# Optimization experiments

Measured on AMD Instinct MI355X. Metric: run time of the kernel, lower is better.

## Reference

```python
import jax, jax.numpy as jnp
import numpy as np

HEADS = 8
DIM_HEAD = 64
NB_FEATURES = 256
CHUNK = 128          # chunk size used by performer's causal_linear_attention_noncuda
EPS_KERNEL = 1e-4    # eps in softmax_kernel feature map
EPS_DENOM = 1e-6     # eps added to k_cumsum in the denominator


def softmax_kernel(data, proj, is_query):
    # FAVOR+ positive softmax random features (performer_pytorch.softmax_kernel)
    # data: [B,H,N,D], proj: [M,D]
    d = data.shape[-1]
    normalizer = d ** -0.25
    ratio = proj.shape[0] ** -0.5
    data_dash = jnp.einsum('bhnd,md->bhnm', data * normalizer, proj)
    # ||x||^2 / (2*sqrt(d))
    diag = jnp.sum(data * data, axis=-1, keepdims=True) * 0.5 * (normalizer ** 2)
    if is_query:
        m = jax.lax.stop_gradient(jnp.max(data_dash, axis=-1, keepdims=True))
    else:
        m = jax.lax.stop_gradient(jnp.max(data_dash, axis=(-1, -2), keepdims=True))
    return ratio * (jnp.exp(data_dash - diag - m) + EPS_KERNEL)


def causal_linear_attention(qp, kp, v, chunk=CHUNK):
    # Chunked causal linear attention (O(N) in seq len):
    # out_i = q'_i . S_i / (q'_i . z_i), S_i = sum_{j<=i} k'_j v_j^T, z_i = cumsum k'_j
    B, H, N, M = qp.shape
    E = v.shape[-1]
    C = N // chunk

    def to_chunks(x):
        return x.reshape(B, H, C, chunk, x.shape[-1]).transpose(2, 0, 1, 3, 4)

    qc, kc, vc = to_chunks(qp), to_chunks(kp), to_chunks(v)
    k0 = jnp.zeros((B, H, M), qp.dtype)
    s0 = jnp.zeros((B, H, M, E), qp.dtype)

    def step(carry, inp):
        k_last, s_last = carry
        q, k, vv = inp  # [B,H,c,M], [B,H,c,M], [B,H,c,E]
        k_cum = k_last[:, :, None, :] + jnp.cumsum(k, axis=2)           # [B,H,c,M]
        d_inv = 1.0 / jnp.einsum('bhnm,bhnm->bhn', q, k_cum + EPS_DENOM)
        ctx = jnp.einsum('bhnm,bhne->bhnme', k, vv)                      # [B,H,c,M,E]
        s_cum = s_last[:, :, None] + jnp.cumsum(ctx, axis=2)             # [B,H,c,M,E]
        out = jnp.einsum('bhnme,bhnm,bhn->bhne', s_cum, q, d_inv)        # [B,H,c,E]
        return (k_cum[:, :, -1, :], s_cum[:, :, -1]), out

    _, outs = jax.lax.scan(step, (k0, s0), (qc, kc, vc))  # [C,B,H,c,E]
    return outs.transpose(1, 2, 0, 3, 4).reshape(B, H, N, E)


def setup_inputs() -> dict:
    key = jax.random.key(0)
    k1, k2, k3, k4 = jax.random.split(key, 4)
    B, N, D = 4, 2048, 512
    return {
        'query': jax.random.normal(k1, (B, N, D), jnp.float32),
        'key': jax.random.normal(k2, (B, N, D), jnp.float32),
        'value': jax.random.normal(k3, (B, N, D), jnp.float32),
        'projection': jax.random.normal(k4, (NB_FEATURES, DIM_HEAD), jnp.float32),
    }


def reference(query, key, value, projection):
    B, N, D = query.shape

    def split(x):  # [B,N,D] -> [B,H,N,Dh]
        return x.reshape(B, N, HEADS, DIM_HEAD).transpose(0, 2, 1, 3)

    q, k, v = split(query), split(key), split(value)
    qp = softmax_kernel(q, projection, is_query=True)
    kp = softmax_kernel(k, projection, is_query=False)
    out = causal_linear_attention(qp, kp, v)
    return out.transpose(0, 2, 1, 3).reshape(B, N, D)
```

## Files before the change

### kernel.cpp

```cpp
#include <hip/hip_runtime.h>
#include <math.h>

#define BB 4
#define NN 2048
#define DD 512
#define HH 8
#define DH 64
#define MM 256
#define BH 32
#define CHK 128
#define NCH 16
#define ROWS (BH*NN)

constexpr float NRM   = 0.35355339059327373f;
constexpr float RATIO = 0.0625f;
constexpr float EPSK  = 1e-4f;
constexpr float EPSD  = 1e-6f;
constexpr float REPS  = 0.0625f * 1e-4f;

#define OFFB_QP   ((size_t)0)
#define OFFB_SP   ((size_t)33554432)
#define OFFB_KP   (OFFB_SP + (size_t)16777216)
#define OFFB_VT   (OFFB_KP + (size_t)33554432)
#define OFFB_Z    (OFFB_VT + (size_t)8388608)
#define OFFB_KMP  (OFFB_Z  + (size_t)524288)
#define OFFB_G    (OFFB_KMP + (size_t)4096)

typedef __attribute__((ext_vector_type(8))) short short8;
typedef __attribute__((ext_vector_type(4))) float f32x4;

__device__ __forceinline__ float b2f(ushort u) {
  union { float f; unsigned int i; } x; x.i = ((unsigned int)u) << 16; return x.f;
}
__device__ __forceinline__ ushort f2b(float f) {
  unsigned int u = __float_as_uint(f);
  unsigned int r = (u + 0x7FFFu + ((u >> 16) & 1u)) >> 16;
  return (ushort)r;
}

#define MFMA(a,b,c) __builtin_amdgcn_mfma_f32_16x16x32_bf16(a, b, c, 0, 0, 0)

template<int MODE>
__device__ __forceinline__ void featm_body(const float* __restrict__ inp,
                                           const float* __restrict__ proj,
                                           char* __restrict__ ws,
                                           char* lds, int blk) {
  ushort* xh = (ushort*)lds;
  ushort* xl = xh + 64*72;
  ushort* qt = (ushort*)lds;
  float* diag_s = (float*)(lds + 33792);
  float (*wmax)[4] = (float(*)[4])(lds + 34048);
  float* kred = (float*)(lds + 35072);

  const int t  = threadIdx.x;
  const int w  = t >> 6;
  const int l  = t & 63;
  const int lq = l >> 4;
  const int ln = l & 15;

  const int rowbase = blk * 64;
  const int bh = rowbase >> 11;
  const int b  = bh >> 3, h = bh & 7;
  const int n0 = rowbase & (NN - 1);

  {
    const int r  = t >> 2;
    const int c0 = (t & 3) * 16;
    const float* src = inp + ((size_t)(b*NN + n0 + r))*DD + h*DH + c0;
    float vv[16];
    #pragma unroll
    for (int j = 0; j < 4; ++j) {
      float4 v = *(const float4*)(src + j*4);
      vv[4*j+0] = v.x*NRM; vv[4*j+1] = v.y*NRM;
      vv[4*j+2] = v.z*NRM; vv[4*j+3] = v.w*NRM;
    }
    float s = 0.f;
    ushort hi[16], lo[16];
    #pragma unroll
    for (int j = 0; j < 16; ++j) {
      s += vv[j]*vv[j];
      hi[j] = f2b(vv[j]);
      lo[j] = f2b(vv[j] - b2f(hi[j]));
    }
    *(short8*)(xh + r*72 + c0)     = *(short8*)&hi[0];
    *(short8*)(xh + r*72 + c0 + 8) = *(short8*)&hi[8];
    *(short8*)(xl + r*72 + c0)     = *(short8*)&lo[0];
    *(short8*)(xl + r*72 + c0 + 8) = *(short8*)&lo[8];
    s += __shfl_xor(s, 1); s += __shfl_xor(s, 2);
    if ((t & 3) == 0) diag_s[r] = 0.5f * s;
  }

  short8 bfr[2][2][2];
  #pragma unroll
  for (int p = 0; p < 2; ++p)
    #pragma unroll
    for (int ntl = 0; ntl < 2; ++ntl) {
      const float* pr = proj + (size_t)(p*128 + w*32 + ntl*16 + ln)*DH;
      #pragma unroll
      for (int kk = 0; kk < 2; ++kk) {
        float4 f0 = *(const float4*)(pr + kk*32 + lq*8);
        float4 f1 = *(const float4*)(pr + kk*32 + lq*8 + 4);
        ushort u[8] = {f2b(f0.x), f2b(f0.y), f2b(f0.z), f2b(f0.w),
                       f2b(f1.x), f2b(f1.y), f2b(f1.z), f2b(f1.w)};
        bfr[p][ntl][kk] = *(short8*)&u[0];
      }
    }

  f32x4 acc[4][4];
  #pragma unroll
  for (int mt = 0; mt < 4; ++mt)
    #pragma unroll
    for (int c = 0; c < 4; ++c) acc[mt][c] = (f32x4){0.f,0.f,0.f,0.f};

  __syncthreads();

  #pragma unroll
  for (int kk = 0; kk < 2; ++kk) {
    short8 ah[4], al[4];
    #pragma unroll
    for (int mt = 0; mt < 4; ++mt) {
      ah[mt] = *(const short8*)(xh + (mt*16 + ln)*72 + kk*32 + lq*8);
      al[mt] = *(const short8*)(xl + (mt*16 + ln)*72 + kk*32 + lq*8);
    }
    #pragma unroll
    for (int p = 0; p < 2; ++p)
      #pragma unroll
      for (int ntl = 0; ntl < 2; ++ntl) {
        short8 bf = bfr[p][ntl][kk];
        #pragma unroll
        for (int mt = 0; mt < 4; ++mt) {
          acc[mt][2*p+ntl] = MFMA(al[mt], bf, acc[mt][2*p+ntl]);
          acc[mt][2*p+ntl] = MFMA(ah[mt], bf, acc[mt][2*p+ntl]);
        }
      }
  }

  if (MODE == 0) {
    #pragma unroll
    for (int mt = 0; mt < 4; ++mt)
      #pragma unroll
      for (int reg = 0; reg < 4; ++reg) {
        float m = acc[mt][0][reg];
        #pragma unroll
        for (int c = 1; c < 4; ++c) m = fmaxf(m, acc[mt][c][reg]);
        m = fmaxf(m, __shfl_xor(m, 1));
        m = fmaxf(m, __shfl_xor(m, 2));
        m = fmaxf(m, __shfl_xor(m, 4));
        m = fmaxf(m, __shfl_xor(m, 8));
        if (ln == 0) wmax[mt*16 + lq*4 + reg][w] = m;
      }
  } else {
    float mx = -1e30f;
    #pragma unroll
    for (int mt = 0; mt < 4; ++mt)
      #pragma unroll
      for (int c = 0; c < 4; ++c)
        #pragma unroll
        for (int reg = 0; reg < 4; ++reg) mx = fmaxf(mx, acc[mt][c][reg]);
    #pragma unroll
    for (int m = 1; m < 64; m <<= 1) mx = fmaxf(mx, __shfl_xor(mx, m));
    if (l == 0) kred[w] = mx;
  }
  __syncthreads();

  float km = 0.f;
  if (MODE == 1) {
    km = fmaxf(fmaxf(kred[0], kred[1]), fmaxf(kred[2], kred[3]));
    if (t == 0) ((float*)(ws + OFFB_KMP))[blk] = km;
  }

  #pragma unroll
  for (int mt = 0; mt < 4; ++mt)
    #pragma unroll
    for (int reg = 0; reg < 4; ++reg) {
      const int row = mt*16 + lq*4 + reg;
      float rm;
      if (MODE == 0) {
        float4 wm4 = *(const float4*)&wmax[row][0];
        rm = fmaxf(fmaxf(wm4.x, wm4.y), fmaxf(wm4.z, wm4.w));
      } else {
        rm = km;
      }
      const float dg = diag_s[row];
      #pragma unroll
      for (int c = 0; c < 4; ++c) {
        const int f = (c >> 1)*128 + w*32 + (c & 1)*16 + ln;
        const float e = __expf(acc[mt][c][reg] - dg - rm);
        qt[row*264 + f] = f2b(MODE == 0 ? RATIO*(e + EPSK) : e);
      }
    }
  __syncthreads();

  ushort* dstbase = (ushort*)(ws + (MODE == 0 ? OFFB_QP : OFFB_KP)) + (size_t)rowbase*MM;
  #pragma unroll
  for (int ld = 0; ld < 8; ++ld) {
    int flat = t + 256*ld;
    int row = flat >> 5, g = flat & 31;
    *(short8*)(dstbase + (size_t)row*MM + g*8) = *(const short8*)(qt + row*264 + g*8);
  }
}

__device__ __forceinline__ void vt_body(const float* __restrict__ value,
                                        char* __restrict__ ws,
                                        char* lds, int blk) {
  float (*vsh)[68] = (float(*)[68])lds;
  const int t = threadIdx.x;
  const int bh = blk >> 4, nc = blk & 15;
  const int b = bh >> 3, h = bh & 7;
  const int n0 = nc * CHK;
  #pragma unroll
  for (int l = 0; l < 8; ++l) {
    int flat = t + 256*l;
    int r = flat >> 4, g = flat & 15;
    *(float4*)&vsh[r][g*4] = *(const float4*)(value + ((size_t)(b*NN + n0 + r))*DD + h*DH + g*4);
  }
  __syncthreads();
  const int e = t & 63, qd = t >> 6;
  ushort* vt = (ushort*)(ws + OFFB_VT) + ((size_t)bh*DH + e)*NN + n0 + qd*32;
  #pragma unroll
  for (int p = 0; p < 16; ++p) {
    unsigned int lo = f2b(vsh[qd*32 + 2*p][e]);
    unsigned int hi = f2b(vsh[qd*32 + 2*p + 1][e]);
    ((unsigned int*)vt)[p] = lo | (hi << 16);
  }
}

__global__ __launch_bounds__(256) void mega_kernel(const float* __restrict__ q,
                                                   const float* __restrict__ k,
                                                   const float* __restrict__ v,
                                                   const float* __restrict__ proj,
                                                   char* __restrict__ ws) {
  __shared__ __align__(16) char lds[35088];
  const int blk = blockIdx.x;
  if (blk < 1024)       featm_body<0>(q, proj, ws, lds, blk);
  else if (blk < 2048)  featm_body<1>(k, proj, ws, lds, blk - 1024);
  else                  vt_body(v, ws, lds, blk - 2048);
}

__global__ __launch_bounds__(256) void gchunk_kernel(char* __restrict__ ws) {
  __shared__ __align__(16) unsigned int kpTh[128*68];
  __shared__ __align__(16) ushort Vts[64*136];

  const int t  = threadIdx.x;
  const int w  = t >> 6;
  const int l  = t & 63;
  const int lq = l >> 4;
  const int ln = l & 15;

  const int blk = blockIdx.x;
  const int mh  = blk & 1;
  const int tc  = (blk >> 1) & 15;
  const int bh  = blk >> 5;

  const float* kmp = (const float*)(ws + OFFB_KMP) + bh*32;
  float km = kmp[0];
  #pragma unroll
  for (int i = 1; i < 32; ++i) km = fmaxf(km, kmp[i]);

  ushort* kpc = (ushort*)(ws + OFFB_KP) + ((size_t)bh*NN + (size_t)tc*CHK)*MM + mh*128;
  const ushort* vtb = (const ushort*)(ws + OFFB_VT) + (size_t)bh*DH*NN + tc*CHK;

  #pragma unroll
  for (int it = 0; it < 4; ++it) {
    int flat = t + 256*it;
    int jp = flat >> 4, mg = flat & 15;
    const float s0 = RATIO * __expf(kmp[tc*2 + (jp >> 5)] - km);
    short8 a = *(const short8*)(kpc + (size_t)(2*jp)*MM + mg*8);
    short8 c = *(const short8*)(kpc + (size_t)(2*jp+1)*MM + mg*8);
    ushort ua[8], uc[8];
    #pragma unroll
    for (int i = 0; i < 8; ++i) {
      ua[i] = f2b(fmaf(b2f((ushort)a[i]), s0, REPS));
      uc[i] = f2b(fmaf(b2f((ushort)c[i]), s0, REPS));
    }
    #pragma unroll
    for (int i = 0; i < 8; ++i)
      kpTh[(mg*8 + i)*68 + jp] = (unsigned int)ua[i] | ((unsigned int)uc[i] << 16);
    *(short8*)(kpc + (size_t)(2*jp)*MM + mg*8)   = *(short8*)&ua[0];
    *(short8*)(kpc + (size_t)(2*jp+1)*MM + mg*8) = *(short8*)&uc[0];
  }
  #pragma unroll
  for (int it = 0; it < 4; ++it) {
    int slot = t + 256*it;
    int e = slot >> 4, g = slot & 15;
    *(short8*)(Vts + e*136 + g*8) = *(const short8*)(vtb + (size_t)e*NN + g*8);
  }
  __syncthreads();

  {
    int m = t >> 1, half = t & 1;
    float s = 0.f;
    #pragma unroll
    for (int u = 0; u < 32; ++u) {
      unsigned int p = kpTh[m*68 + half*32 + u];
      s += b2f((ushort)(p & 0xFFFF)) + b2f((ushort)(p >> 16));
    }
    s += __shfl_xor(s, 1);
    if (half == 0)
      ((float*)(ws + OFFB_Z))[((size_t)bh*NCH + tc)*MM + mh*128 + m] = s;
  }

  f32x4 acc[8];
  #pragma unroll
  for (int nt = 0; nt < 8; ++nt) acc[nt] = (f32x4){0.f,0.f,0.f,0.f};
  short8 af[4];
  #pragma unroll
  for (int kk = 0; kk < 4; ++kk)
    af[kk] = *(const short8*)(Vts + (w*16 + ln)*136 + kk*32 + lq*8);
  #pragma unroll
  for (int nt = 0; nt < 8; ++nt)
    #pragma unroll
    for (int kk = 0; kk < 4; ++kk) {
      short8 bf = *(const short8*)((const ushort*)kpTh + (size_t)(nt*16 + ln)*136 + kk*32 + lq*8);
      acc[nt] = MFMA(af[kk], bf, acc[nt]);
    }

  float* gb = (float*)(ws + OFFB_G) + ((size_t)bh*NCH + tc)*DH*MM + mh*128;
  #pragma unroll
  for (int nt = 0; nt < 8; ++nt)
    #pragma unroll
    for (int reg = 0; reg < 4; ++reg)
      gb[(size_t)(w*16 + lq*4 + reg)*MM + nt*16 + ln] = acc[nt][reg];
}

__global__ __launch_bounds__(256) void scan_kernel(char* __restrict__ ws) {
  const int t  = threadIdx.x;
  const int bh = blockIdx.x / 17;
  const int sl = blockIdx.x % 17;
  if (sl < 16) {
    const int e  = sl*4 + (t >> 6);
    const int m4 = (t & 63) * 4;
    const float* gb = (const float*)(ws + OFFB_G) + ((size_t)bh*NCH*DH + e)*MM + m4;
    ushort*     spb = (ushort*)(ws + OFFB_SP)     + ((size_t)bh*NCH*DH + e)*MM + m4;
    float4 g[NCH];
    #pragma unroll
    for (int tc = 0; tc < NCH; ++tc)
      g[tc] = *(const float4*)(gb + (size_t)tc*DH*MM);
    float4 acc = {0.f, 0.f, 0.f, 0.f};
    #pragma unroll
    for (int tc = 0; tc < NCH; ++tc) {
      ushort4 o;
      o.x = f2b(acc.x); o.y = f2b(acc.y); o.z = f2b(acc.z); o.w = f2b(acc.w);
      *(ushort4*)(spb + (size_t)tc*DH*MM) = o;
      acc.x += g[tc].x; acc.y += g[tc].y; acc.z += g[tc].z; acc.w += g[tc].w;
    }
  } else {
    float* zf = (float*)(ws + OFFB_Z) + (size_t)bh*NCH*MM + t;
    float g[NCH];
    #pragma unroll
    for (int tc = 0; tc < NCH; ++tc) g[tc] = zf[(size_t)tc*MM];
    float acc = 0.f;
    #pragma unroll
    for (int tc = 0; tc < NCH; ++tc) { zf[(size_t)tc*MM] = acc; acc += g[tc]; }
  }
}

__global__ __launch_bounds__(256) void fused_kernel(float* __restrict__ out,
                                                    char* __restrict__ ws) {
  __shared__ __align__(16) char lds[52224];
  __shared__ float den_i[128];
  __shared__ float dinv_s[128];

  const int t  = threadIdx.x;
  const int w  = t >> 6;
  const int l  = t & 63;
  const int lq = l >> 4;
  const int ln = l & 15;
  const int rt0 = w;
  const int rt1 = 7 - w;
  const int blk = blockIdx.x;
  const int bh = blk >> 4, tc = blk & 15;
  const int b = bh >> 3, h = bh & 7;
  const size_t rowbase = (size_t)bh*NN + tc*CHK;

  const ushort* qpg = (const ushort*)(ws + OFFB_QP) + rowbase*MM;
  const ushort* kpg = (const ushort*)(ws + OFFB_KP) + rowbase*MM;
  const ushort* spg = (const ushort*)(ws + OFFB_SP) + (size_t)blk*DH*MM;

  ushort* qs = (ushort*)lds;
  ushort* ks = qs + 128*72;
  ushort* ss = ks + 128*72;

  f32x4 acc[2][8];
  #pragma unroll
  for (int mt = 0; mt < 2; ++mt)
    #pragma unroll
    for (int nt = 0; nt < 8; ++nt) acc[mt][nt] = (f32x4){0.f,0.f,0.f,0.f};
  f32x4 oacc[2][4];
  #pragma unroll
  for (int mt = 0; mt < 2; ++mt)
    #pragma unroll
    for (int nt = 0; nt < 4; ++nt) oacc[mt][nt] = (f32x4){0.f,0.f,0.f,0.f};

  for (int mc = 0; mc < 4; ++mc) {
    __syncthreads();
    #pragma unroll
    for (int ld2 = 0; ld2 < 4; ++ld2) {
      int flat = t + 256*ld2; int r = flat >> 3, g = flat & 7;
      *(short8*)(qs + r*72 + g*8) = *(const short8*)(qpg + (size_t)r*MM + mc*64 + g*8);
    }
    #pragma unroll
    for (int ld2 = 0; ld2 < 4; ++ld2) {
      int flat = t + 256*ld2; int r = flat >> 3, g = flat & 7;
      *(short8*)(ks + r*72 + g*8) = *(const short8*)(kpg + (size_t)r*MM + mc*64 + g*8);
    }
    #pragma unroll
    for (int ld2 = 0; ld2 < 2; ++ld2) {
      int flat = t + 256*ld2; int e = flat >> 3, g = flat & 7;
      *(short8*)(ss + e*72 + g*8) = *(const short8*)(spg + (size_t)e*MM + mc*64 + g*8);
    }
    __syncthreads();
    #pragma unroll
    for (int kk = 0; kk < 2; ++kk) {
      short8 af0 = *(const short8*)(qs + (rt0*16 + ln)*72 + kk*32 + lq*8);
      short8 af1 = *(const short8*)(qs + (rt1*16 + ln)*72 + kk*32 + lq*8);
      #pragma unroll
      for (int nt = 0; nt < 8; ++nt) {
        if (nt <= rt1) {
          short8 bf = *(const short8*)(ks + (nt*16 + ln)*72 + kk*32 + lq*8);
          if (nt <= rt0) acc[0][nt] = MFMA(af0, bf, acc[0][nt]);
          acc[1][nt] = MFMA(af1, bf, acc[1][nt]);
        }
      }
      #pragma unroll
      for (int nt = 0; nt < 4; ++nt) {
        short8 bf = *(const short8*)(ss + (nt*16 + ln)*72 + kk*32 + lq*8);
        oacc[0][nt] = MFMA(af0, bf, oacc[0][nt]);
        oacc[1][nt] = MFMA(af1, bf, oacc[1][nt]);
      }
    }
  }

  __syncthreads();

  ushort* P   = (ushort*)lds;
  ushort* Vts = (ushort*)(lds + 34816);

  float rs[2][4] = {{0,0,0,0},{0,0,0,0}};
  #pragma unroll
  for (int mt = 0; mt < 2; ++mt) {
    const int ibase = (mt ? rt1 : rt0) * 16;
    #pragma unroll
    for (int nt = 0; nt < 8; ++nt)
      #pragma unroll
      for (int reg = 0; reg < 4; ++reg) {
        int i = ibase + lq*4 + reg;
        int j = nt*16 + ln;
        float v = (j <= i) ? acc[mt][nt][reg] : 0.f;
        rs[mt][reg] += v;
        P[i*136 + j] = f2b(v);
      }
  }
  #pragma unroll
  for (int mt = 0; mt < 2; ++mt) {
    const int ibase = (mt ? rt1 : rt0) * 16;
    #pragma unroll
    for (int reg = 0; reg < 4; ++reg) {
      float s = rs[mt][reg];
      s += __shfl_xor(s, 1); s += __shfl_xor(s, 2);
      s += __shfl_xor(s, 4); s += __shfl_xor(s, 8);
      if (ln == 0) den_i[ibase + lq*4 + reg] = s;
    }
  }

  const ushort* vtg = (const ushort*)(ws + OFFB_VT) + (size_t)bh*DH*NN + tc*CHK;
  #pragma unroll
  for (int ld2 = 0; ld2 < 4; ++ld2) {
    int flat = t + 256*ld2; int e = flat >> 4, g = flat & 15;
    *(short8*)(Vts + e*136 + g*8) = *(const short8*)(vtg + (size_t)e*NN + g*8);
  }
  __syncthreads();

  {
    const float* zp = (const float*)(ws + OFFB_Z) + (size_t)blk*MM;
    const int r = t >> 1, hf = t & 1;
    const ushort* qrow = qpg + (size_t)r*MM + hf*128;
    float s = 0.f;
    #pragma unroll
    for (int g = 0; g < 16; ++g) {
      short8 qv = *(const short8*)(qrow + g*8);
      const float* zz = zp + hf*128 + g*8;
      #pragma unroll
      for (int x = 0; x < 8; ++x)
        s += b2f((ushort)qv[x]) * (zz[x] + EPSD);
    }
    s += __shfl_xor(s, 1);
    if (hf == 0) dinv_s[r] = 1.0f / (s + den_i[r]);
  }
  __syncthreads();

  #pragma unroll
  for (int kk = 0; kk < 4; ++kk) {
    short8 af0 = *(const short8*)(P + (rt0*16 + ln)*136 + kk*32 + lq*8);
    short8 af1 = *(const short8*)(P + (rt1*16 + ln)*136 + kk*32 + lq*8);
    #pragma unroll
    for (int nt = 0; nt < 4; ++nt) {
      short8 bf = *(const short8*)(Vts + (nt*16 + ln)*136 + kk*32 + lq*8);
      oacc[0][nt] = MFMA(af0, bf, oacc[0][nt]);
      oacc[1][nt] = MFMA(af1, bf, oacc[1][nt]);
    }
  }

  #pragma unroll
  for (int mt = 0; mt < 2; ++mt) {
    const int ibase = (mt ? rt1 : rt0) * 16;
    #pragma unroll
    for (int reg = 0; reg < 4; ++reg) {
      const int i = ibase + lq*4 + reg;
      const float di = dinv_s[i];
      float* dst = out + ((size_t)(b*NN) + tc*CHK + i)*DD + h*DH;
      #pragma unroll
      for (int nt = 0; nt < 4; ++nt)
        dst[nt*16 + ln] = oacc[mt][nt][reg] * di;
    }
  }
}

extern "C" void kernel_launch(void* const* d_in, const int* in_sizes, int n_in,
                              void* d_out, int out_size, void* d_ws, size_t ws_size,
                              hipStream_t stream) {
  (void)in_sizes; (void)n_in; (void)out_size; (void)ws_size;
  const float* q    = (const float*)d_in[0];
  const float* k    = (const float*)d_in[1];
  const float* v    = (const float*)d_in[2];
  const float* proj = (const float*)d_in[3];
  float* out = (float*)d_out;
  char*  ws  = (char*)d_ws;

  mega_kernel<<<2560, 256, 0, stream>>>(q, k, v, proj, ws);
  gchunk_kernel<<<1024, 256, 0, stream>>>(ws);
  scan_kernel<<<544, 256, 0, stream>>>(ws);
  fused_kernel<<<512, 256, 0, stream>>>(out, ws);
}
```

Measured before the change: 187.5 us.

## Drop scaled k' writeback, rescale in fused kernel, prefetch tiles into registers

The earlier kernel no longer writes the max-rescaled bf16 k' back to global memory. Instead, the fused kernel recomputes the per-chunk scale from the stored maxima and applies it while staging k' into LDS. The fused kernel also prefetches the next q/k/S column slice into registers during the MFMA loop, giving software pipelining of global loads. It computes the q·z denominator during staging, reusing loaded q values instead of re-reading q' from global memory. This removes global write and read traffic but adds register pressure, which may lower occupancy.

After: 168.3 us. 10.2% less time.

```diff
diff --git a/kernel.cpp b/kernel.cpp
--- a/kernel.cpp
+++ b/kernel.cpp
@@ -257,7 +257,7 @@
   #pragma unroll
   for (int i = 1; i < 32; ++i) km = fmaxf(km, kmp[i]);
 
-  ushort* kpc = (ushort*)(ws + OFFB_KP) + ((size_t)bh*NN + (size_t)tc*CHK)*MM + mh*128;
+  const ushort* kpc = (const ushort*)(ws + OFFB_KP) + ((size_t)bh*NN + (size_t)tc*CHK)*MM + mh*128;
   const ushort* vtb = (const ushort*)(ws + OFFB_VT) + (size_t)bh*DH*NN + tc*CHK;
 
   #pragma unroll
@@ -276,8 +276,6 @@
     #pragma unroll
     for (int i = 0; i < 8; ++i)
       kpTh[(mg*8 + i)*68 + jp] = (unsigned int)ua[i] | ((unsigned int)uc[i] << 16);
-    *(short8*)(kpc + (size_t)(2*jp)*MM + mg*8)   = *(short8*)&ua[0];
-    *(short8*)(kpc + (size_t)(2*jp+1)*MM + mg*8) = *(short8*)&uc[0];
   }
   #pragma unroll
   for (int it = 0; it < 4; ++it) {
@@ -359,6 +357,7 @@
                                                     char* __restrict__ ws) {
   __shared__ __align__(16) char lds[52224];
   __shared__ float den_i[128];
+  __shared__ float den_q[128];
   __shared__ float dinv_s[128];
 
   const int t  = threadIdx.x;
@@ -377,9 +376,38 @@
   const ushort* kpg = (const ushort*)(ws + OFFB_KP) + rowbase*MM;
   const ushort* spg = (const ushort*)(ws + OFFB_SP) + (size_t)blk*DH*MM;
 
+  const float* kmp = (const float*)(ws + OFFB_KMP) + bh*32;
+  float km = kmp[0];
+  #pragma unroll
+  for (int i = 1; i < 32; ++i) km = fmaxf(km, kmp[i]);
+  const float sc0 = RATIO * __expf(kmp[tc*2]     - km);
+  const float sc1 = RATIO * __expf(kmp[tc*2 + 1] - km);
+
   ushort* qs = (ushort*)lds;
   ushort* ks = qs + 128*72;
   ushort* ss = ks + 128*72;
+  float*  zl = (float*)(lds + 46080);
+
+  {
+    const float* zp = (const float*)(ws + OFFB_Z) + (size_t)blk*MM;
+    zl[t] = zp[t] + EPSD;
+  }
+
+  const int r4 = t >> 3;
+  const int g8 = t & 7;
+
+  short8 rq[4], rk[4], rs2[2];
+  #pragma unroll
+  for (int ld2 = 0; ld2 < 4; ++ld2)
+    rq[ld2] = *(const short8*)(qpg + (size_t)(r4 + 32*ld2)*MM + g8*8);
+  #pragma unroll
+  for (int ld2 = 0; ld2 < 4; ++ld2)
+    rk[ld2] = *(const short8*)(kpg + (size_t)(r4 + 32*ld2)*MM + g8*8);
+  #pragma unroll
+  for (int ld2 = 0; ld2 < 2; ++ld2)
+    rs2[ld2] = *(const short8*)(spg + (size_t)(r4 + 32*ld2)*MM + g8*8);
+
+  float dp[4] = {0.f, 0.f, 0.f, 0.f};
 
   f32x4 acc[2][8];
   #pragma unroll
@@ -396,20 +424,39 @@
     __syncthreads();
     #pragma unroll
     for (int ld2 = 0; ld2 < 4; ++ld2) {
-      int flat = t + 256*ld2; int r = flat >> 3, g = flat & 7;
-      *(short8*)(qs + r*72 + g*8) = *(const short8*)(qpg + (size_t)r*MM + mc*64 + g*8);
+      const int r = r4 + 32*ld2;
+      *(short8*)(qs + r*72 + g8*8) = rq[ld2];
+      #pragma unroll
+      for (int i = 0; i < 8; ++i)
+        dp[ld2] += b2f((ushort)rq[ld2][i]) * zl[mc*64 + g8*8 + i];
     }
     #pragma unroll
     for (int ld2 = 0; ld2 < 4; ++ld2) {
-      int flat = t + 256*ld2; int r = flat >> 3, g = flat & 7;
-      *(short8*)(ks + r*72 + g*8) = *(const short8*)(kpg + (size_t)r*MM + mc*64 + g*8);
-    }
-    #pragma unroll
-    for (int ld2 = 0; ld2 < 2; ++ld2) {
-      int flat = t + 256*ld2; int e = flat >> 3, g = flat & 7;
-      *(short8*)(ss + e*72 + g*8) = *(const short8*)(spg + (size_t)e*MM + mc*64 + g*8);
-    }
+      const int r = r4 + 32*ld2;
+      const float sc = (r & 64) ? sc1 : sc0;
+      ushort ov[8];
+      #pragma unroll
+      for (int i = 0; i < 8; ++i) ov[i] = f2b(fmaf(b2f((ushort)rk[ld2][i]), sc, REPS));
+      *(short8*)(ks + r*72 + g8*8) = *(short8*)&ov[0];
+    }
+    #pragma unroll
+    for (int ld2 = 0; ld2 < 2; ++ld2)
+      *(short8*)(ss + (r4 + 32*ld2)*72 + g8*8) = rs2[ld2];
     __syncthreads();
+
+    if (mc < 3) {
+      const int c0 = (mc + 1) * 64;
+      #pragma unroll
+      for (int ld2 = 0; ld2 < 4; ++ld2)
+        rq[ld2] = *(const short8*)(qpg + (size_t)(r4 + 32*ld2)*MM + c0 + g8*8);
+      #pragma unroll
+      for (int ld2 = 0; ld2 < 4; ++ld2)
+        rk[ld2] = *(const short8*)(kpg + (size_t)(r4 + 32*ld2)*MM + c0 + g8*8);
+      #pragma unroll
+      for (int ld2 = 0; ld2 < 2; ++ld2)
+        rs2[ld2] = *(const short8*)(spg + (size_t)(r4 + 32*ld2)*MM + c0 + g8*8);
+    }
+
     #pragma unroll
     for (int kk = 0; kk < 2; ++kk) {
       short8 af0 = *(const short8*)(qs + (rt0*16 + ln)*72 + kk*32 + lq*8);
@@ -431,6 +478,13 @@
     }
   }
 
+  #pragma unroll
+  for (int ld2 = 0; ld2 < 4; ++ld2) {
+    float s = dp[ld2];
+    s += __shfl_xor(s, 1); s += __shfl_xor(s, 2); s += __shfl_xor(s, 4);
+    if (g8 == 0) den_q[r4 + 32*ld2] = s;
+  }
+
   __syncthreads();
 
   ushort* P   = (ushort*)lds;
@@ -471,22 +525,7 @@
   }
   __syncthreads();
 
-  {
-    const float* zp = (const float*)(ws + OFFB_Z) + (size_t)blk*MM;
-    const int r = t >> 1, hf = t & 1;
-    const ushort* qrow = qpg + (size_t)r*MM + hf*128;
-    float s = 0.f;
-    #pragma unroll
-    for (int g = 0; g < 16; ++g) {
-      short8 qv = *(const short8*)(qrow + g*8);
-      const float* zz = zp + hf*128 + g*8;
-      #pragma unroll
-      for (int x = 0; x < 8; ++x)
-        s += b2f((ushort)qv[x]) * (zz[x] + EPSD);
-    }
-    s += __shfl_xor(s, 1);
-    if (hf == 0) dinv_s[r] = 1.0f / (s + den_i[r]);
-  }
+  if (t < 128) dinv_s[t] = 1.0f / (den_q[t] + den_i[t]);
   __syncthreads();
 
   #pragma unroll
```

## Fuse key rescaling into attention kernel, widen to 512 threads, prefetch tiles

Applied to the files above, without the earlier changes.

Stops gchunk_kernel from writing the rescaled bf16 key features back to global memory. fused_kernel now applies the per-chunk scale to keys while staging them into LDS. fused_kernel moves to 512 threads with one 16-row tile per wave, register-prefetches the next q/k/S slices during MFMA work, and folds the query·z denominator into the staging loop. mega_kernel gets an occupancy hint. This removes a global write pass and the separate denominator pass, at the cost of redundant scaling work and higher register pressure.

Result: faster. 174.5 us (-7.0%).

```diff
diff --git a/kernel.cpp b/kernel.cpp
--- a/kernel.cpp
+++ b/kernel.cpp
@@ -225,11 +225,11 @@
   }
 }
 
-__global__ __launch_bounds__(256) void mega_kernel(const float* __restrict__ q,
-                                                   const float* __restrict__ k,
-                                                   const float* __restrict__ v,
-                                                   const float* __restrict__ proj,
-                                                   char* __restrict__ ws) {
+__global__ __launch_bounds__(256, 3) void mega_kernel(const float* __restrict__ q,
+                                                      const float* __restrict__ k,
+                                                      const float* __restrict__ v,
+                                                      const float* __restrict__ proj,
+                                                      char* __restrict__ ws) {
   __shared__ __align__(16) char lds[35088];
   const int blk = blockIdx.x;
   if (blk < 1024)       featm_body<0>(q, proj, ws, lds, blk);
@@ -257,7 +257,7 @@
   #pragma unroll
   for (int i = 1; i < 32; ++i) km = fmaxf(km, kmp[i]);
 
-  ushort* kpc = (ushort*)(ws + OFFB_KP) + ((size_t)bh*NN + (size_t)tc*CHK)*MM + mh*128;
+  const ushort* kpc = (const ushort*)(ws + OFFB_KP) + ((size_t)bh*NN + (size_t)tc*CHK)*MM + mh*128;
   const ushort* vtb = (const ushort*)(ws + OFFB_VT) + (size_t)bh*DH*NN + tc*CHK;
 
   #pragma unroll
@@ -276,8 +276,6 @@
     #pragma unroll
     for (int i = 0; i < 8; ++i)
       kpTh[(mg*8 + i)*68 + jp] = (unsigned int)ua[i] | ((unsigned int)uc[i] << 16);
-    *(short8*)(kpc + (size_t)(2*jp)*MM + mg*8)   = *(short8*)&ua[0];
-    *(short8*)(kpc + (size_t)(2*jp+1)*MM + mg*8) = *(short8*)&uc[0];
   }
   #pragma unroll
   for (int it = 0; it < 4; ++it) {
@@ -355,10 +353,11 @@
   }
 }
 
-__global__ __launch_bounds__(256) void fused_kernel(float* __restrict__ out,
-                                                    char* __restrict__ ws) {
+__global__ __launch_bounds__(512, 4) void fused_kernel(float* __restrict__ out,
+                                                       char* __restrict__ ws) {
   __shared__ __align__(16) char lds[52224];
   __shared__ float den_i[128];
+  __shared__ float den_q[128];
   __shared__ float dinv_s[128];
 
   const int t  = threadIdx.x;
@@ -366,8 +365,7 @@
   const int l  = t & 63;
   const int lq = l >> 4;
   const int ln = l & 15;
-  const int rt0 = w;
-  const int rt1 = 7 - w;
+  const int rt = w;
   const int blk = blockIdx.x;
   const int bh = blk >> 4, tc = blk & 15;
   const int b = bh >> 3, h = bh & 7;
@@ -377,58 +375,96 @@
   const ushort* kpg = (const ushort*)(ws + OFFB_KP) + rowbase*MM;
   const ushort* spg = (const ushort*)(ws + OFFB_SP) + (size_t)blk*DH*MM;
 
+  const float* kmp = (const float*)(ws + OFFB_KMP) + bh*32;
+  float km = kmp[0];
+  #pragma unroll
+  for (int i = 1; i < 32; ++i) km = fmaxf(km, kmp[i]);
+  const float sc0 = RATIO * __expf(kmp[tc*2]     - km);
+  const float sc1 = RATIO * __expf(kmp[tc*2 + 1] - km);
+
   ushort* qs = (ushort*)lds;
   ushort* ks = qs + 128*72;
   ushort* ss = ks + 128*72;
-
-  f32x4 acc[2][8];
-  #pragma unroll
-  for (int mt = 0; mt < 2; ++mt)
-    #pragma unroll
-    for (int nt = 0; nt < 8; ++nt) acc[mt][nt] = (f32x4){0.f,0.f,0.f,0.f};
-  f32x4 oacc[2][4];
-  #pragma unroll
-  for (int mt = 0; mt < 2; ++mt)
-    #pragma unroll
-    for (int nt = 0; nt < 4; ++nt) oacc[mt][nt] = (f32x4){0.f,0.f,0.f,0.f};
+  float*  zl = (float*)(lds + 46080);
+
+  if (t < 256) {
+    const float* zp = (const float*)(ws + OFFB_Z) + (size_t)blk*MM;
+    zl[t] = zp[t] + EPSD;
+  }
+
+  const int r8 = t >> 3;
+  const int g8 = t & 7;
+
+  short8 rq[2], rk[2], rs1;
+  rq[0] = *(const short8*)(qpg + (size_t)(r8     )*MM + g8*8);
+  rq[1] = *(const short8*)(qpg + (size_t)(r8 + 64)*MM + g8*8);
+  rk[0] = *(const short8*)(kpg + (size_t)(r8     )*MM + g8*8);
+  rk[1] = *(const short8*)(kpg + (size_t)(r8 + 64)*MM + g8*8);
+  rs1   = *(const short8*)(spg + (size_t)r8*MM + g8*8);
+
+  float dp[2] = {0.f, 0.f};
+
+  f32x4 acc[8];
+  #pragma unroll
+  for (int nt = 0; nt < 8; ++nt) acc[nt] = (f32x4){0.f,0.f,0.f,0.f};
+  f32x4 oacc[4];
+  #pragma unroll
+  for (int nt = 0; nt < 4; ++nt) oacc[nt] = (f32x4){0.f,0.f,0.f,0.f};
 
   for (int mc = 0; mc < 4; ++mc) {
     __syncthreads();
-    #pragma unroll
-    for (int ld2 = 0; ld2 < 4; ++ld2) {
-      int flat = t + 256*ld2; int r = flat >> 3, g = flat & 7;
-      *(short8*)(qs + r*72 + g*8) = *(const short8*)(qpg + (size_t)r*MM + mc*64 + g*8);
-    }
-    #pragma unroll
-    for (int ld2 = 0; ld2 < 4; ++ld2) {
-      int flat = t + 256*ld2; int r = flat >> 3, g = flat & 7;
-      *(short8*)(ks + r*72 + g*8) = *(const short8*)(kpg + (size_t)r*MM + mc*64 + g*8);
-    }
-    #pragma unroll
-    for (int ld2 = 0; ld2 < 2; ++ld2) {
-      int flat = t + 256*ld2; int e = flat >> 3, g = flat & 7;
-      *(short8*)(ss + e*72 + g*8) = *(const short8*)(spg + (size_t)e*MM + mc*64 + g*8);
-    }
+    *(short8*)(qs + (r8     )*72 + g8*8) = rq[0];
+    *(short8*)(qs + (r8 + 64)*72 + g8*8) = rq[1];
+    #pragma unroll
+    for (int i = 0; i < 2; ++i)
+      #pragma unroll
+      for (int j = 0; j < 8; ++j)
+        dp[i] += b2f((ushort)rq[i][j]) * zl[mc*64 + g8*8 + j];
+    {
+      ushort ov0[8], ov1[8];
+      #pragma unroll
+      for (int j = 0; j < 8; ++j) {
+        ov0[j] = f2b(fmaf(b2f((ushort)rk[0][j]), sc0, REPS));
+        ov1[j] = f2b(fmaf(b2f((ushort)rk[1][j]), sc1, REPS));
+      }
+      *(short8*)(ks + (r8     )*72 + g8*8) = *(short8*)&ov0[0];
+      *(short8*)(ks + (r8 + 64)*72 + g8*8) = *(short8*)&ov1[0];
+    }
+    *(short8*)(ss + r8*72 + g8*8) = rs1;
     __syncthreads();
+
+    if (mc < 3) {
+      const int c0 = (mc + 1) * 64;
+      rq[0] = *(const short8*)(qpg + (size_t)(r8     )*MM + c0 + g8*8);
+      rq[1] = *(const short8*)(qpg + (size_t)(r8 + 64)*MM + c0 + g8*8);
+      rk[0] = *(const short8*)(kpg + (size_t)(r8     )*MM + c0 + g8*8);
+      rk[1] = *(const short8*)(kpg + (size_t)(r8 + 64)*MM + c0 + g8*8);
+      rs1   = *(const short8*)(spg + (size_t)r8*MM + c0 + g8*8);
+    }
+
     #pragma unroll
     for (int kk = 0; kk < 2; ++kk) {
-      short8 af0 = *(const short8*)(qs + (rt0*16 + ln)*72 + kk*32 + lq*8);
-      short8 af1 = *(const short8*)(qs + (rt1*16 + ln)*72 + kk*32 + lq*8);
+      short8 af = *(const short8*)(qs + (rt*16 + ln)*72 + kk*32 + lq*8);
       #pragma unroll
       for (int nt = 0; nt < 8; ++nt) {
-        if (nt <= rt1) {
+        if (nt <= rt) {
           short8 bf = *(const short8*)(ks + (nt*16 + ln)*72 + kk*32 + lq*8);
-          if (nt <= rt0) acc[0][nt] = MFMA(af0, bf, acc[0][nt]);
-          acc[1][nt] = MFMA(af1, bf, acc[1][nt]);
+          acc[nt] = MFMA(af, bf, acc[nt]);
         }
       }
       #pragma unroll
       for (int nt = 0; nt < 4; ++nt) {
         short8 bf = *(const short8*)(ss + (nt*16 + ln)*72 + kk*32 + lq*8);
-        oacc[0][nt] = MFMA(af0, bf, oacc[0][nt]);
-        oacc[1][nt] = MFMA(af1, bf, oacc[1][nt]);
-      }
-    }
+        oacc[nt] = MFMA(af, bf, oacc[nt]);
+      }
+    }
+  }
+
+  #pragma unroll
+  for (int i = 0; i < 2; ++i) {
+    float s = dp[i];
+    s += __shfl_xor(s, 1); s += __shfl_xor(s, 2); s += __shfl_xor(s, 4);
+    if (g8 == 0) den_q[r8 + 64*i] = s;
   }
 
   __syncthreads();
@@ -436,83 +472,58 @@
   ushort* P   = (ushort*)lds;
   ushort* Vts = (ushort*)(lds + 34816);
 
-  float rs[2][4] = {{0,0,0,0},{0,0,0,0}};
-  #pragma unroll
-  for (int mt = 0; mt < 2; ++mt) {
-    const int ibase = (mt ? rt1 : rt0) * 16;
+  {
+    float rsv[4] = {0.f, 0.f, 0.f, 0.f};
     #pragma unroll
     for (int nt = 0; nt < 8; ++nt)
       #pragma unroll
       for (int reg = 0; reg < 4; ++reg) {
-        int i = ibase + lq*4 + reg;
+        int i = rt*16 + lq*4 + reg;
         int j = nt*16 + ln;
-        float v = (j <= i) ? acc[mt][nt][reg] : 0.f;
-        rs[mt][reg] += v;
+        float v = (j <= i) ? acc[nt][reg] : 0.f;
+        rsv[reg] += v;
         P[i*136 + j] = f2b(v);
       }
-  }
-  #pragma unroll
-  for (int mt = 0; mt < 2; ++mt) {
-    const int ibase = (mt ? rt1 : rt0) * 16;
     #pragma unroll
     for (int reg = 0; reg < 4; ++reg) {
-      float s = rs[mt][reg];
+      float s = rsv[reg];
       s += __shfl_xor(s, 1); s += __shfl_xor(s, 2);
       s += __shfl_xor(s, 4); s += __shfl_xor(s, 8);
-      if (ln == 0) den_i[ibase + lq*4 + reg] = s;
-    }
-  }
-
-  const ushort* vtg = (const ushort*)(ws + OFFB_VT) + (size_t)bh*DH*NN + tc*CHK;
-  #pragma unroll
-  for (int ld2 = 0; ld2 < 4; ++ld2) {
-    int flat = t + 256*ld2; int e = flat >> 4, g = flat & 15;
-    *(short8*)(Vts + e*136 + g*8) = *(const short8*)(vtg + (size_t)e*NN + g*8);
-  }
-  __syncthreads();
+      if (ln == 0) den_i[rt*16 + lq*4 + reg] = s;
+    }
+  }
 
   {
-    const float* zp = (const float*)(ws + OFFB_Z) + (size_t)blk*MM;
-    const int r = t >> 1, hf = t & 1;
-    const ushort* qrow = qpg + (size_t)r*MM + hf*128;
-    float s = 0.f;
-    #pragma unroll
-    for (int g = 0; g < 16; ++g) {
-      short8 qv = *(const short8*)(qrow + g*8);
-      const float* zz = zp + hf*128 + g*8;
-      #pragma unroll
-      for (int x = 0; x < 8; ++x)
-        s += b2f((ushort)qv[x]) * (zz[x] + EPSD);
-    }
-    s += __shfl_xor(s, 1);
-    if (hf == 0) dinv_s[r] = 1.0f / (s + den_i[r]);
-  }
+    const ushort* vtg = (const ushort*)(ws + OFFB_VT) + (size_t)bh*DH*NN + tc*CHK;
+    #pragma unroll
+    for (int it = 0; it < 2; ++it) {
+      int slot = t + 512*it; int e = slot >> 4, g = slot & 15;
+      *(short8*)(Vts + e*136 + g*8) = *(const short8*)(vtg + (size_t)e*NN + g*8);
+    }
+  }
+  __syncthreads();
+
+  if (t < 128) dinv_s[t] = 1.0f / (den_q[t] + den_i[t]);
   __syncthreads();
 
   #pragma unroll
   for (int kk = 0; kk < 4; ++kk) {
-    short8 af0 = *(const short8*)(P + (rt0*16 + ln)*136 + kk*32 + lq*8);
-    short8 af1 = *(const short8*)(P + (rt1*16 + ln)*136 + kk*32 + lq*8);
+    short8 af = *(const short8*)(P + (rt*16 + ln)*136 + kk*32 + lq*8);
     #pragma unroll
     for (int nt = 0; nt < 4; ++nt) {
       short8 bf = *(const short8*)(Vts + (nt*16 + ln)*136 + kk*32 + lq*8);
-      oacc[0][nt] = MFMA(af0, bf, oacc[0][nt]);
-      oacc[1][nt] = MFMA(af1, bf, oacc[1][nt]);
-    }
-  }
-
-  #pragma unroll
-  for (int mt = 0; mt < 2; ++mt) {
-    const int ibase = (mt ? rt1 : rt0) * 16;
-    #pragma unroll
-    for (int reg = 0; reg < 4; ++reg) {
-      const int i = ibase + lq*4 + reg;
-      const float di = dinv_s[i];
-      float* dst = out + ((size_t)(b*NN) + tc*CHK + i)*DD + h*DH;
-      #pragma unroll
-      for (int nt = 0; nt < 4; ++nt)
-        dst[nt*16 + ln] = oacc[mt][nt][reg] * di;
-    }
+      oacc[nt] = MFMA(af, bf, oacc[nt]);
+    }
+  }
+
+  #pragma unroll
+  for (int reg = 0; reg < 4; ++reg) {
+    const int i = rt*16 + lq*4 + reg;
+    const float di = dinv_s[i];
+    float* dst = out + ((size_t)(b*NN) + tc*CHK + i)*DD + h*DH;
+    #pragma unroll
+    for (int nt = 0; nt < 4; ++nt)
+      dst[nt*16 + ln] = oacc[nt][reg] * di;
   }
 }
 
@@ -530,5 +541,5 @@
   mega_kernel<<<2560, 256, 0, stream>>>(q, k, v, proj, ws);
   gchunk_kernel<<<1024, 256, 0, stream>>>(ws);
   scan_kernel<<<544, 256, 0, stream>>>(ws);
-  fused_kernel<<<512, 256, 0, stream>>>(out, ws);
-}
+  fused_kernel<<<512, 512, 0, stream>>>(out, ws);
+}
```
